# Optimization experiments

Measured on AMD Instinct MI355X. Metric: run time of the kernel, lower is better.

Reference implementation:

```python
import jax, jax.numpy as jnp
import numpy as np

N_NODES = 50000
EMBED_DIM = 100
N_RAND_EDGES = 600000
NEG_SLOPE = 0.2  # alpha in the original module


def _build_pairs(n_nodes, n_edges, seed=0):
    """Replicates: neighbors(v) = unique(out_nbrs(v) U in_nbrs(v)) for all v,
    flattened into (seg=v, nbr=u) pair arrays (symmetrized, deduped edge list)."""
    rng = np.random.default_rng(seed)
    src = rng.integers(0, n_nodes, n_edges)
    dst = rng.integers(0, n_nodes, n_edges)
    ring = np.arange(n_nodes)  # guarantee every node has a neighbor
    src = np.concatenate([src, ring])
    dst = np.concatenate([dst, (ring + 1) % n_nodes])
    seg = np.concatenate([src, dst])
    nbr = np.concatenate([dst, src])
    pairs = np.unique(np.stack([seg, nbr], axis=1), axis=0)  # sorted by seg
    return pairs[:, 0].astype(np.int32), pairs[:, 1].astype(np.int32)


def setup_inputs() -> dict:
    key = jax.random.key(0)
    k1, k2 = jax.random.split(key)
    hidden = jax.random.normal(k1, (N_NODES, EMBED_DIM), dtype=jnp.float32)
    # nn.Linear(embed_dim, 1, bias=False) weight, kaiming-uniform-ish scale
    W = jax.random.normal(k2, (EMBED_DIM,), dtype=jnp.float32) / np.sqrt(EMBED_DIM)
    seg_np, nbr_np = _build_pairs(N_NODES, N_RAND_EDGES)
    return {"hidden": hidden, "W": W,
            "seg": jnp.asarray(seg_np), "nbr": jnp.asarray(nbr_np)}


def reference(hidden, W, seg, nbr):
    n = hidden.shape[0]
    h_i = hidden[seg]            # [P, D] center node repeated per neighbor
    h_j = hidden[nbr]            # [P, D] gathered neighbor embeddings
    scores = jnp.einsum('pd,d->p', h_i * h_j, W)           # a(neighbors*hidden)
    scores = jnp.where(scores >= 0, scores, NEG_SLOPE * scores)  # leaky_relu
    # per-node (segment) softmax, numerically stable
    m = jax.ops.segment_max(scores, seg, num_segments=n)
    e = jnp.exp(scores - m[seg])
    z = jax.ops.segment_sum(e, seg, num_segments=n)
    alpha = e / z[seg]                                      # [P]
    out = jax.ops.segment_sum(alpha[:, None] * h_j, seg, num_segments=n)  # [N, D]
    return out
```

## Files before the change

### kernel.cpp

```cpp
#include <hip/hip_runtime.h>
#include <math.h>

#define D 100
#define NEG_SLOPE 0.2f
#define CHUNK 16
#define ROWU 52
#define NPB 2

#define COMPILER_FENCE() asm volatile("" ::: "memory")

typedef _Float16 f16x2 __attribute__((ext_vector_type(2)));
union U32H2 { unsigned int u; f16x2 h; };

__device__ __forceinline__ unsigned int pkh2(float x, float y) {
    U32H2 c; c.h.x = (_Float16)x; c.h.y = (_Float16)y; return c.u;
}

__device__ __forceinline__ float dot2u(unsigned int au, unsigned int xu, float acc) {
#if __has_builtin(__builtin_amdgcn_fdot2)
    U32H2 a, x; a.u = au; x.u = xu;
    return __builtin_amdgcn_fdot2(a.h, x.h, acc, false);
#else
    U32H2 a, x; a.u = au; x.u = xu;
    return acc + (float)a.h.x * (float)x.h.x + (float)a.h.y * (float)x.h.y;
#endif
}

template<int CTRL>
__device__ __forceinline__ float dppf(float x) {
    return __uint_as_float((unsigned)__builtin_amdgcn_update_dpp(
        0, (int)__float_as_uint(x), CTRL, 0xF, 0xF, true));
}
__device__ __forceinline__ float red16_max(float x) {
    x = fmaxf(x, dppf<0xB1>(x));
    x = fmaxf(x, dppf<0x4E>(x));
    x = fmaxf(x, dppf<0x124>(x));
    x = fmaxf(x, dppf<0x128>(x));
    return x;
}
__device__ __forceinline__ float red16_sum(float x) {
    x += dppf<0xB1>(x);
    x += dppf<0x4E>(x);
    x += dppf<0x124>(x);
    x += dppf<0x128>(x);
    return x;
}

__global__ void prep_kernel(const int* __restrict__ seg,
                            int* __restrict__ row_ptr,
                            const float* __restrict__ hidden,
                            unsigned int* __restrict__ hb,
                            int n, int P, int total25)
{
    int t = blockIdx.x * blockDim.x + threadIdx.x;
    if (t < P) {
        int s0 = seg[t];
        if (t == 0)
            for (int v = 0; v <= s0; v++) row_ptr[v] = 0;
        int s1 = (t + 1 < P) ? seg[t + 1] : n;
        for (int v = s0 + 1; v <= s1; v++) row_ptr[v] = t + 1;
    }
    if (t < total25) {
        int node = t / 25, k = t - node * 25;
        float4 f = ((const float4*)hidden)[t];
        *(uint2*)&hb[node * ROWU + 2 * k] =
            make_uint2(pkh2(f.x, f.y), pkh2(f.z, f.w));
    }
}

#define ACCU4(b, X) do {                                                      \
    U32H2 t_;                                                                 \
    t_.u = (X).x; accA[(b)+0] = fmaf((float)t_.h.x, e, accA[(b)+0]);          \
                  accA[(b)+1] = fmaf((float)t_.h.y, e, accA[(b)+1]);          \
    t_.u = (X).y; accA[(b)+2] = fmaf((float)t_.h.x, e, accA[(b)+2]);          \
                  accA[(b)+3] = fmaf((float)t_.h.y, e, accA[(b)+3]);          \
    t_.u = (X).z; accA[(b)+4] = fmaf((float)t_.h.x, e, accA[(b)+4]);          \
                  accA[(b)+5] = fmaf((float)t_.h.y, e, accA[(b)+5]);          \
    t_.u = (X).w; accA[(b)+6] = fmaf((float)t_.h.x, e, accA[(b)+6]);          \
                  accA[(b)+7] = fmaf((float)t_.h.y, e, accA[(b)+7]);          \
} while (0)

__launch_bounds__(64 * NPB, 6)
__global__ void gat_agg_kernel(const float* __restrict__ hidden,
                               const float* __restrict__ W,
                               const int* __restrict__ nbr,
                               const int* __restrict__ row_ptr,
                               const unsigned int* __restrict__ hb,
                               float* __restrict__ out,
                               int n, int P)
{
    __shared__ __align__(16) unsigned int s_hwp[NPB][ROWU];

    const int lane = threadIdx.x & 63;
    const int wid  = threadIdx.x >> 6;
    const int v    = blockIdx.x * NPB + wid;
    if (v >= n) return;

    if (lane < 50) {
        float2 h2 = ((const float2*)(hidden + (long)v * D))[lane];
        float2 w2 = ((const float2*)W)[lane];
        s_hwp[wid][lane] = pkh2(h2.x * w2.x, h2.y * w2.y);
    }
    COMPILER_FENCE();

    const int start = row_ptr[v];
    const int end   = row_ptr[v + 1];

    if (end <= start) {
        if (lane < D / 2)
            ((float2*)(out + (long)v * D))[lane] = make_float2(0.f, 0.f);
        return;
    }

    const int q  = lane >> 4;
    const int jl = lane & 15;
    const int t0 = q * 3;

    const uint4* hwq = ((const uint4*)&s_hwp[wid][0]) + t0;
    const uint4 a0 = hwq[0], a1 = hwq[1], a2 = hwq[2];
    uint2 at = make_uint2(0u, 0u);
    if (q == 0) at = *(const uint2*)&s_hwp[wid][48];

    float accA[24];
    float accT[4];
    #pragma unroll
    for (int i = 0; i < 24; ++i) accA[i] = 0.f;
    #pragma unroll
    for (int i = 0; i < 4; ++i) accT[i] = 0.f;

    float m = -INFINITY, z = 0.f;

    for (int c = start; c < end; c += CHUNK) {
        const int  cnt = min(CHUNK, end - c);
        const bool pv  = jl < cnt;

        const int nbv = pv ? nbr[c + jl] : 0;
        const uint4* row16 = ((const uint4*)hb) + nbv * (ROWU / 4) + t0;

        uint4 x0 = row16[0], x1 = row16[1], x2 = row16[2];
        uint2 xt = make_uint2(0u, 0u);
        if (q == 0) xt = *(const uint2*)&hb[nbv * ROWU + 48];

        float p0 = 0.f, p1 = 0.f, p2 = 0.f, p3 = 0.f;
        p0 = dot2u(a0.x, x0.x, p0);  p1 = dot2u(a0.y, x0.y, p1);
        p2 = dot2u(a0.z, x0.z, p2);  p3 = dot2u(a0.w, x0.w, p3);
        p0 = dot2u(a1.x, x1.x, p0);  p1 = dot2u(a1.y, x1.y, p1);
        p2 = dot2u(a1.z, x1.z, p2);  p3 = dot2u(a1.w, x1.w, p3);
        p0 = dot2u(a2.x, x2.x, p0);  p1 = dot2u(a2.y, x2.y, p1);
        p2 = dot2u(a2.z, x2.z, p2);  p3 = dot2u(a2.w, x2.w, p3);
        if (q == 0) {
            p0 = dot2u(at.x, xt.x, p0);
            p1 = dot2u(at.y, xt.y, p1);
        }

        float part = (p0 + p1) + (p2 + p3);
        part += __shfl_xor(part, 16, 64);
        part += __shfl_xor(part, 32, 64);
        const float s = pv ? (part >= 0.f ? part : NEG_SLOPE * part)
                           : -INFINITY;

        const float m_new = fmaxf(m, red16_max(s));
        const float e     = pv ? __expf(s - m_new) : 0.f;
        const float gsum  = red16_sum(e);

        if (m_new != m) {
            const float scale = __expf(m - m_new);
            z *= scale;
            #pragma unroll
            for (int i = 0; i < 24; ++i) accA[i] *= scale;
            #pragma unroll
            for (int i = 0; i < 4; ++i) accT[i] *= scale;
            m = m_new;
        }
        z += gsum;

        ACCU4(0,  x0);
        ACCU4(8,  x1);
        ACCU4(16, x2);
        if (q == 0) {
            U32H2 t_;
            t_.u = xt.x; accT[0] = fmaf((float)t_.h.x, e, accT[0]);
                         accT[1] = fmaf((float)t_.h.y, e, accT[1]);
            t_.u = xt.y; accT[2] = fmaf((float)t_.h.x, e, accT[2]);
                         accT[3] = fmaf((float)t_.h.y, e, accT[3]);
        }
    }

    #pragma unroll
    for (int i = 0; i < 24; ++i) accA[i] = red16_sum(accA[i]);
    #pragma unroll
    for (int i = 0; i < 4; ++i) accT[i] = red16_sum(accT[i]);

    const float inv = 1.f / z;
    float2* orow = (float2*)(out + (long)v * D);
    #pragma unroll
    for (int j = 0; j < 12; ++j) {
        if (jl == j)
            orow[q * 12 + j] = make_float2(accA[2 * j] * inv,
                                           accA[2 * j + 1] * inv);
    }
    if (lane == 12) orow[48] = make_float2(accT[0] * inv, accT[1] * inv);
    if (lane == 13) orow[49] = make_float2(accT[2] * inv, accT[3] * inv);
}

extern "C" void kernel_launch(void* const* d_in, const int* in_sizes, int n_in,
                              void* d_out, int out_size, void* d_ws, size_t ws_size,
                              hipStream_t stream) {
    const float* hidden = (const float*)d_in[0];
    const float* W      = (const float*)d_in[1];
    const int*   seg    = (const int*)d_in[2];
    const int*   nbr    = (const int*)d_in[3];
    float*       out    = (float*)d_out;

    const int Ddim = in_sizes[1];
    const int n    = in_sizes[0] / Ddim;
    const int P    = in_sizes[2];

    int* row_ptr = (int*)d_ws;
    size_t hb_off = (((size_t)(n + 1) * 4) + 255) & ~(size_t)255;
    unsigned int* hb = (unsigned int*)((char*)d_ws + hb_off);

    const int total25 = n * 25;
    const int tmax    = (P > total25) ? P : total25;
    hipLaunchKernelGGL(prep_kernel, dim3((tmax + 255) / 256), dim3(256), 0, stream,
                       seg, row_ptr, hidden, hb, n, P, total25);
    hipLaunchKernelGGL(gat_agg_kernel, dim3((n + NPB - 1) / NPB), dim3(64 * NPB),
                       0, stream, hidden, W, nbr, row_ptr, hb, out, n, P);
}
```

Baseline: 141.4 us.

## Replace per-element 16-lane accumulator reductions with recursive-halving transpose reduction

The epilogue used to run a full 16-lane DPP sum on each of the 24 accumulators, then had one lane per slot write out a float2. It now does a recursive-halving butterfly. At each step lanes swap halves of their accumulator set, so every lane ends up owning a few finished outputs, which cuts the number of DPP/shuffle ops and moves from serialized float2 stores to scalar stores spread across lanes. The launch-bounds occupancy hint also goes from 6 to 8 waves, which may limit registers and risk spills.

```diff
diff --git a/kernel.cpp b/kernel.cpp
--- a/kernel.cpp
+++ b/kernel.cpp
@@ -80,7 +80,7 @@
                   accA[(b)+7] = fmaf((float)t_.h.y, e, accA[(b)+7]);          \
 } while (0)
 
-__launch_bounds__(64 * NPB, 6)
+__launch_bounds__(64 * NPB, 8)
 __global__ void gat_agg_kernel(const float* __restrict__ hidden,
                                const float* __restrict__ W,
                                const int* __restrict__ nbr,
@@ -186,21 +186,53 @@
         }
     }
 
-    #pragma unroll
-    for (int i = 0; i < 24; ++i) accA[i] = red16_sum(accA[i]);
-    #pragma unroll
-    for (int i = 0; i < 4; ++i) accT[i] = red16_sum(accT[i]);
-
     const float inv = 1.f / z;
-    float2* orow = (float2*)(out + (long)v * D);
+    float* orow = out + (long)v * D;
+
+    const float T0 = red16_sum(accT[0]) * inv;
+    const float T1 = red16_sum(accT[1]) * inv;
+    const float T2 = red16_sum(accT[2]) * inv;
+    const float T3 = red16_sum(accT[3]) * inv;
+    if (lane == 0) ((float2*)orow)[48] = make_float2(T0, T1);
+    if (lane == 1) ((float2*)orow)[49] = make_float2(T2, T3);
+
+    const bool b8 = (jl & 8) != 0;
+    const bool b4 = (jl & 4) != 0;
+    const bool b2 = (jl & 2) != 0;
+    const bool b1 = (jl & 1) != 0;
+
+    float w[12];
     #pragma unroll
     for (int j = 0; j < 12; ++j) {
-        if (jl == j)
-            orow[q * 12 + j] = make_float2(accA[2 * j] * inv,
-                                           accA[2 * j + 1] * inv);
-    }
-    if (lane == 12) orow[48] = make_float2(accT[0] * inv, accT[1] * inv);
-    if (lane == 13) orow[49] = make_float2(accT[2] * inv, accT[3] * inv);
+        const float lo = accA[j], hi = accA[j + 12];
+        w[j] = (b8 ? hi : lo) + dppf<0x128>(b8 ? lo : hi);
+    }
+    float u[6];
+    #pragma unroll
+    for (int j = 0; j < 6; ++j) {
+        const float lo = w[j], hi = w[j + 6];
+        u[j] = (b2 ? hi : lo) + dppf<0x4E>(b2 ? lo : hi);
+    }
+    float r0, r1, r2;
+    {
+        const float l0 = u[0], h0 = u[3];
+        r0 = (b1 ? h0 : l0) + dppf<0xB1>(b1 ? l0 : h0);
+        const float l1 = u[1], h1 = u[4];
+        r1 = (b1 ? h1 : l1) + dppf<0xB1>(b1 ? l1 : h1);
+        const float l2 = u[2], h2 = u[5];
+        r2 = (b1 ? h2 : l2) + dppf<0xB1>(b1 ? l2 : h2);
+    }
+    r0 += __shfl_xor(r0, 4, 64);
+    r1 += __shfl_xor(r1, 4, 64);
+    r2 += __shfl_xor(r2, 4, 64);
+
+    const int base = 24 * q + (b8 ? 12 : 0) + (b2 ? 6 : 0) + (b1 ? 3 : 0);
+    if (!b4) {
+        orow[base]     = r0 * inv;
+        orow[base + 1] = r1 * inv;
+    } else {
+        orow[base + 2] = r2 * inv;
+    }
 }
 
 extern "C" void kernel_launch(void* const* d_in, const int* in_sizes, int n_in,
```

Measured after the change: 220.5 us. 55.9% more time.
